# Kernel optimization log

Measured on AMD Instinct MI355X. Metric: run time of the kernel, lower is better.

Reference implementation:

```python
import math
import jax, jax.numpy as jnp
import numpy as np

D_MODEL, N_HEADS, D_FF = 2048, 16, 8192
B, T = 4, 1024
D_HEAD = D_MODEL // N_HEADS
LN_EPS = 1e-5


def hadamard(x):
    """Orthonormal Hadamard transform along last dim (power-of-two length)."""
    n = x.shape[-1]
    y = x.reshape(-1, n)
    h = 1
    while h < n:
        y = y.reshape(-1, n // (2 * h), 2, h)
        a, b = y[..., 0, :], y[..., 1, :]
        y = jnp.concatenate([a + b, a - b], axis=-1).reshape(-1, n)
        h *= 2
    return (y / math.sqrt(n)).reshape(x.shape)


def quantize_int8_per_row(W):
    s = jnp.maximum(jnp.max(jnp.abs(W), axis=1, keepdims=True), 1e-8) / 127.0
    Q = jnp.clip(jnp.round(W / s), -127, 127).astype(jnp.int8)
    return Q, s


def make_dtdr_weight(key, out_f, in_f):
    W = jax.random.normal(key, (out_f, in_f), dtype=jnp.float32) * 0.02
    return quantize_int8_per_row(hadamard(W))  # W_tilde = W @ H, then int8


def setup_inputs() -> dict:
    key = jax.random.key(0)
    ks = jax.random.split(key, 8)
    x = jax.random.normal(ks[0], (B, T, D_MODEL), dtype=jnp.float32)
    Qq, sq = make_dtdr_weight(ks[1], D_MODEL, D_MODEL)
    Qk, sk = make_dtdr_weight(ks[2], D_MODEL, D_MODEL)
    Qv, sv = make_dtdr_weight(ks[3], D_MODEL, D_MODEL)
    Qo, so = make_dtdr_weight(ks[4], D_MODEL, D_MODEL)
    Qf1, sf1 = make_dtdr_weight(ks[5], D_FF, D_MODEL)
    Qf2, sf2 = make_dtdr_weight(ks[6], D_MODEL, D_FF)
    return dict(
        x=x,
        ln1_g=jnp.ones((D_MODEL,), jnp.float32), ln1_b=jnp.zeros((D_MODEL,), jnp.float32),
        ln2_g=jnp.ones((D_MODEL,), jnp.float32), ln2_b=jnp.zeros((D_MODEL,), jnp.float32),
        Qq=Qq, sq=sq, Qk=Qk, sk=sk, Qv=Qv, sv=sv, Qo=Qo, so=so,
        Qf1=Qf1, sf1=sf1, bf1=jnp.zeros((D_FF,), jnp.float32),
        Qf2=Qf2, sf2=sf2, bf2=jnp.zeros((D_MODEL,), jnp.float32),
    )


def layernorm(x, g, b):
    mu = jnp.mean(x, axis=-1, keepdims=True)
    var = jnp.mean(jnp.square(x - mu), axis=-1, keepdims=True)
    return (x - mu) / jnp.sqrt(var + LN_EPS) * g + b


def dtdr_linear(x, Q, s, bias=None):
    # y = (H x) @ dequant(Q)^T + b
    xh = hadamard(x.astype(jnp.float32))
    W = Q.astype(jnp.float32) * s  # (out, in)
    y = jnp.einsum('btd,od->bto', xh, W)
    return y if bias is None else y + bias


def reference(x, ln1_g, ln1_b, ln2_g, ln2_b, Qq, sq, Qk, sk, Qv, sv, Qo, so,
              Qf1, sf1, bf1, Qf2, sf2, bf2):
    Bc, Tc, C = x.shape
    h = layernorm(x, ln1_g, ln1_b)
    q = dtdr_linear(h, Qq, sq).reshape(Bc, Tc, N_HEADS, D_HEAD).transpose(0, 2, 1, 3)
    k = dtdr_linear(h, Qk, sk).reshape(Bc, Tc, N_HEADS, D_HEAD).transpose(0, 2, 1, 3)
    v = dtdr_linear(h, Qv, sv).reshape(Bc, Tc, N_HEADS, D_HEAD).transpose(0, 2, 1, 3)
    scores = jnp.einsum('bhqd,bhkd->bhqk', q, k) / math.sqrt(D_HEAD)
    p = jax.nn.softmax(scores, axis=-1)
    out = jnp.einsum('bhqk,bhkd->bhqd', p, v)
    out = out.transpose(0, 2, 1, 3).reshape(Bc, Tc, C)
    x = x + dtdr_linear(out, Qo, so)
    h = layernorm(x, ln2_g, ln2_b)
    ff = dtdr_linear(h, Qf1, sf1, bf1)
    ff = jax.nn.gelu(ff, approximate=False)  # torch F.gelu default = erf gelu
    x = x + dtdr_linear(ff, Qf2, sf2, bf2)
    return x
```

## Files before the change

kernel.cpp:

```cpp
#include <hip/hip_runtime.h>
#include <cstdint>
#include <cstddef>

typedef unsigned short u16;
typedef unsigned int   u32;
typedef __bf16 bf16x8 __attribute__((ext_vector_type(8)));
typedef float  f32x4  __attribute__((ext_vector_type(4)));

__device__ __forceinline__ float bf2f(u16 u) {
  union { u32 i; float f; } v; v.i = ((u32)u) << 16; return v.f;
}
__device__ __forceinline__ u16 f2bf(float f) {
  union { float f; u32 i; } v; v.f = f;
  u32 r = v.i + 0x7fffu + ((v.i >> 16) & 1u);
  return (u16)(r >> 16);
}
__device__ __forceinline__ void unpack8(uint4 raw, float* v) {
  v[0]=bf2f(raw.x&0xffff); v[1]=bf2f(raw.x>>16);
  v[2]=bf2f(raw.y&0xffff); v[3]=bf2f(raw.y>>16);
  v[4]=bf2f(raw.z&0xffff); v[5]=bf2f(raw.z>>16);
  v[6]=bf2f(raw.w&0xffff); v[7]=bf2f(raw.w>>16);
}
__device__ __forceinline__ uint4 pack8(const float* v) {
  uint4 r;
  r.x = (u32)f2bf(v[0]) | ((u32)f2bf(v[1])<<16);
  r.y = (u32)f2bf(v[2]) | ((u32)f2bf(v[3])<<16);
  r.z = (u32)f2bf(v[4]) | ((u32)f2bf(v[5])<<16);
  r.w = (u32)f2bf(v[6]) | ((u32)f2bf(v[7])<<16);
  return r;
}
__device__ __forceinline__ void gload16(const void* g, void* l) {
  __builtin_amdgcn_global_load_lds((const __attribute__((address_space(1))) void*)g,
                                   (__attribute__((address_space(3))) void*)l, 16, 0, 0);
}

template<typename T>
__device__ __forceinline__ void load8(const T* p, float* v);
template<> __device__ __forceinline__ void load8<float>(const float* p, float* v) {
  const float4 a = ((const float4*)p)[0];
  const float4 b = ((const float4*)p)[1];
  v[0]=a.x; v[1]=a.y; v[2]=a.z; v[3]=a.w;
  v[4]=b.x; v[5]=b.y; v[6]=b.z; v[7]=b.w;
}
template<> __device__ __forceinline__ void load8<u16>(const u16* p, float* v) {
  unpack8(*(const uint4*)p, v);
}

__global__ __launch_bounds__(256) void cvt_k(const int* __restrict__ Q, u16* __restrict__ W) {
  const size_t i = ((size_t)blockIdx.x * 256 + threadIdx.x) * 8;
  const int4 a = *(const int4*)(Q + i);
  const int4 b = *(const int4*)(Q + i + 4);
  union { float f; u32 u; } c;
  uint4 r;
  u32 t;
  c.f = (float)a.x; t = c.u >> 16; c.f = (float)a.y; r.x = t | (c.u & 0xffff0000u);
  c.f = (float)a.z; t = c.u >> 16; c.f = (float)a.w; r.y = t | (c.u & 0xffff0000u);
  c.f = (float)b.x; t = c.u >> 16; c.f = (float)b.y; r.z = t | (c.u & 0xffff0000u);
  c.f = (float)b.z; t = c.u >> 16; c.f = (float)b.w; r.w = t | (c.u & 0xffff0000u);
  *(uint4*)(W + i) = r;
}

template<typename T>
__global__ __launch_bounds__(256) void ln_fwht_k(const T* __restrict__ X,
    const float* __restrict__ G, const float* __restrict__ Bt, u16* __restrict__ O) {
  __shared__ float buf[2048];
  __shared__ float red[8];
  const int tid = threadIdx.x;
  const int lane = tid & 63, wave = tid >> 6;
  const size_t base = (size_t)blockIdx.x * 2048;
  float v[8]; load8(X + base + tid*8, v);
  float s = 0.f, s2 = 0.f;
  for (int j = 0; j < 8; ++j) { s += v[j]; s2 += v[j]*v[j]; }
  for (int m = 1; m < 64; m <<= 1) { s += __shfl_xor(s, m, 64); s2 += __shfl_xor(s2, m, 64); }
  if (lane == 0) { red[wave] = s; red[4 + wave] = s2; }
  __syncthreads();
  s  = red[0] + red[1] + red[2] + red[3];
  s2 = red[4] + red[5] + red[6] + red[7];
  const float mu = s * (1.f/2048.f);
  const float rstd = rsqrtf(s2 * (1.f/2048.f) - mu*mu + 1e-5f);
  float g[8], bb[8];
  load8(G + tid*8, g); load8(Bt + tid*8, bb);
  for (int j = 0; j < 8; ++j) buf[tid*8 + j] = (v[j] - mu) * rstd * g[j] + bb[j];
  __syncthreads();
  for (int h = 1; h < 2048; h <<= 1) {
    for (int p = 0; p < 4; ++p) {
      const int idx = p*256 + tid;
      const int i = ((idx & ~(h-1)) << 1) | (idx & (h-1));
      const float a = buf[i], c = buf[i + h];
      buf[i] = a + c; buf[i + h] = a - c;
    }
    __syncthreads();
  }
  float o[8];
  for (int j = 0; j < 8; ++j) o[j] = buf[tid*8 + j] * 0.02209708691207961f;
  *(uint4*)&O[base + tid*8] = pack8(o);
}

template<int N>
__global__ __launch_bounds__(256) void fwht_ip(u16* __restrict__ D) {
  __shared__ float buf[N];
  const int tid = threadIdx.x;
  const size_t base = (size_t)blockIdx.x * N;
  constexpr int V8 = N / (8*256);
  for (int i = 0; i < V8; ++i) {
    uint4 raw = *(const uint4*)&D[base + (i*256 + tid)*8];
    float v[8]; unpack8(raw, v);
    for (int j = 0; j < 8; ++j) buf[(i*256 + tid)*8 + j] = v[j];
  }
  __syncthreads();
  constexpr int PAIRS = N / 2 / 256;
  for (int h = 1; h < N; h <<= 1) {
    for (int p = 0; p < PAIRS; ++p) {
      const int idx = p*256 + tid;
      const int i = ((idx & ~(h-1)) << 1) | (idx & (h-1));
      const float a = buf[i], c = buf[i + h];
      buf[i] = a + c; buf[i + h] = a - c;
    }
    __syncthreads();
  }
  const float sc = rsqrtf((float)N);
  for (int i = 0; i < V8; ++i) {
    float v[8];
    for (int j = 0; j < 8; ++j) v[j] = buf[(i*256 + tid)*8 + j] * sc;
    *(uint4*)&D[base + (i*256 + tid)*8] = pack8(v);
  }
}

__global__ __launch_bounds__(256, 2) void gemm_bt(
    const u16* __restrict__ A, const u16* __restrict__ Bw, const float* __restrict__ S,
    void* __restrict__ C, int ldc, int M, int N, int K,
    const float* __restrict__ bias, const float* __restrict__ resf,
    const u16* __restrict__ resb, int dogelu, int outf32)
{
  __shared__ alignas(16) u16 sA[2][128*32];
  __shared__ alignas(16) u16 sB[2][128*32];
  const int tid = threadIdx.x;
  const int lane = tid & 63, wave = tid >> 6;
  const int quad = lane >> 4, l16 = lane & 15;
  const int wm = wave & 1, wn = wave >> 1;
  const int nwg = gridDim.x * gridDim.y;
  int flat = blockIdx.y * gridDim.x + blockIdx.x;
  if ((nwg & 7) == 0) flat = (flat & 7) * (nwg >> 3) + (flat >> 3);
  const long tM = (long)(flat % gridDim.x) * 128;
  const long tN = (long)(flat / gridDim.x) * 128;
  const int sr = lane >> 2;
  const int scol = (lane & 3) * 8;
  const u16* a0 = A  + (size_t)(tM + wave*16      + sr)*K + scol;
  const u16* a1 = A  + (size_t)(tM + (wave+4)*16  + sr)*K + scol;
  const u16* b0 = Bw + (size_t)(tN + wave*16      + sr)*K + scol;
  const u16* b1 = Bw + (size_t)(tN + (wave+4)*16  + sr)*K + scol;

  auto stage = [&](int buf, int k0) {
    gload16(a0 + k0, &sA[buf][ wave   *512]);
    gload16(a1 + k0, &sA[buf][(wave+4)*512]);
    gload16(b0 + k0, &sB[buf][ wave   *512]);
    gload16(b1 + k0, &sB[buf][(wave+4)*512]);
  };

  f32x4 acc[4][4] = {};
  auto compute = [&](int buf) {
    bf16x8 af[4], bq[4];
#pragma unroll
    for (int t = 0; t < 4; ++t) af[t] = *(const bf16x8*)&sA[buf][(wm*64 + t*16 + l16)*32 + quad*8];
#pragma unroll
    for (int t = 0; t < 4; ++t) bq[t] = *(const bf16x8*)&sB[buf][(wn*64 + t*16 + l16)*32 + quad*8];
#pragma unroll
    for (int im = 0; im < 4; ++im)
#pragma unroll
      for (int in = 0; in < 4; ++in)
        acc[im][in] = __builtin_amdgcn_mfma_f32_16x16x32_bf16(af[im], bq[in], acc[im][in], 0, 0, 0);
  };

  const int nk = K >> 5;
  stage(0, 0);
  __syncthreads();
  int cur = 0;
  for (int t = 0; t < nk - 1; ++t) {
    stage(cur ^ 1, (t + 1) << 5);
    compute(cur);
    __syncthreads();
    cur ^= 1;
  }
  compute(cur);

#pragma unroll
  for (int in = 0; in < 4; ++in) {
    const long col = tN + wn*64 + in*16 + l16;
    const float sc = S[col];
    const float bv = bias ? bias[col] : 0.f;
#pragma unroll
    for (int im = 0; im < 4; ++im) {
      const long row0 = tM + wm*64 + im*16 + quad*4;
#pragma unroll
      for (int r = 0; r < 4; ++r) {
        float v = acc[im][in][r] * sc + bv;
        if (dogelu) v = 0.5f * v * (1.f + erff(v * 0.7071067811865475f));
        const size_t off = (size_t)(row0 + r)*ldc + col;
        if (resf) v += resf[off];
        if (resb) v += bf2f(resb[off]);
        if (outf32) ((float*)C)[off] = v;
        else        ((u16*)C)[off]   = f2bf(v);
      }
    }
  }
}

__global__ __launch_bounds__(256, 2) void attn_k(const u16* __restrict__ QKV, u16* __restrict__ O)
{
  __shared__ alignas(16) u16 sKV[16384];
  __shared__ alignas(16) u16 sP[16384];
  const int tid = threadIdx.x;
  const int lane = tid & 63, wave = tid >> 6;
  const int quad = lane >> 4, l16 = lane & 15;
  const int qt = blockIdx.x;
  const int bh = blockIdx.y;
  const int b = bh >> 4, h = bh & 15;
  const size_t rb = (size_t)b * 1024;
  const u16* Qg = QKV + (rb + (size_t)qt*128)*6144 + h*128;
  const u16* Kg = QKV + rb*6144 + 2048 + h*128;
  const u16* Vg = QKV + rb*6144 + 4096 + h*128;

  for (int c = 0; c < 8; ++c) {
    const int chunk = c*4 + wave;
    const int r = chunk*4 + quad;
    gload16(Qg + (size_t)r*6144 + l16*8, &sP[chunk*512]);
  }
  __syncthreads();
  bf16x8 aq[2][4];
  for (int im = 0; im < 2; ++im)
    for (int kk = 0; kk < 4; ++kk)
      aq[im][kk] = *(const bf16x8*)&sP[(wave*32 + im*16 + l16)*128 + kk*32 + quad*8];

  float mrun[2][4], lrun[2][4];
  f32x4 oacc[2][8] = {};
  for (int im = 0; im < 2; ++im)
    for (int r = 0; r < 4; ++r) { mrun[im][r] = -1e30f; lrun[im][r] = 0.f; }

  for (int kt = 0; kt < 8; ++kt) {
    __syncthreads();
    for (int c = 0; c < 8; ++c) {
      const int chunk = c*4 + wave;
      const int r = chunk*4 + quad;
      gload16(Kg + (size_t)(kt*128 + r)*6144 + l16*8, &sKV[chunk*512]);
    }
    __syncthreads();
    f32x4 sf[2][8] = {};
#pragma unroll
    for (int kk = 0; kk < 4; ++kk)
#pragma unroll
      for (int jn = 0; jn < 8; ++jn) {
        const bf16x8 bk = *(const bf16x8*)&sKV[(jn*16 + l16)*128 + kk*32 + quad*8];
        sf[0][jn] = __builtin_amdgcn_mfma_f32_16x16x32_bf16(aq[0][kk], bk, sf[0][jn], 0, 0, 0);
        sf[1][jn] = __builtin_amdgcn_mfma_f32_16x16x32_bf16(aq[1][kk], bk, sf[1][jn], 0, 0, 0);
      }
    const float scale = 0.08838834764831845f;
#pragma unroll
    for (int im = 0; im < 2; ++im)
#pragma unroll
      for (int r = 0; r < 4; ++r) {
        float mx = -1e30f;
        for (int jn = 0; jn < 8; ++jn) mx = fmaxf(mx, sf[im][jn][r] * scale);
        for (int m = 1; m < 16; m <<= 1) mx = fmaxf(mx, __shfl_xor(mx, m, 64));
        const float mold = mrun[im][r];
        const float mnew = fmaxf(mold, mx);
        const float alpha = __expf(mold - mnew);
        float ls = 0.f;
        for (int jn = 0; jn < 8; ++jn) {
          const float p = __expf(sf[im][jn][r] * scale - mnew);
          ls += p;
          sP[wave*4096 + (im*16 + quad*4 + r)*128 + jn*16 + l16] = f2bf(p);
        }
        for (int m = 1; m < 16; m <<= 1) ls += __shfl_xor(ls, m, 64);
        lrun[im][r] = lrun[im][r]*alpha + ls;
        mrun[im][r] = mnew;
        for (int od = 0; od < 8; ++od) oacc[im][od][r] *= alpha;
      }
    __syncthreads();
    for (int c = 0; c < 8; ++c) {
      const int chunk = c*256 + tid;
      const int kv = chunk >> 4;
      const int db = (chunk & 15) * 8;
      const uint4 raw = *(const uint4*)(Vg + (size_t)(kt*128 + kv)*6144 + db);
      const u32 w0[4] = {raw.x, raw.y, raw.z, raw.w};
      for (int j = 0; j < 4; ++j) {
        sKV[(db + 2*j  )*128 + kv] = (u16)(w0[j] & 0xffff);
        sKV[(db + 2*j+1)*128 + kv] = (u16)(w0[j] >> 16);
      }
    }
    __syncthreads();
#pragma unroll
    for (int kk = 0; kk < 4; ++kk) {
      const bf16x8 ap0 = *(const bf16x8*)&sP[wave*4096 + (     l16)*128 + kk*32 + quad*8];
      const bf16x8 ap1 = *(const bf16x8*)&sP[wave*4096 + (16 + l16)*128 + kk*32 + quad*8];
#pragma unroll
      for (int od = 0; od < 8; ++od) {
        const bf16x8 bv = *(const bf16x8*)&sKV[(od*16 + l16)*128 + kk*32 + quad*8];
        oacc[0][od] = __builtin_amdgcn_mfma_f32_16x16x32_bf16(ap0, bv, oacc[0][od], 0, 0, 0);
        oacc[1][od] = __builtin_amdgcn_mfma_f32_16x16x32_bf16(ap1, bv, oacc[1][od], 0, 0, 0);
      }
    }
  }
  for (int im = 0; im < 2; ++im)
    for (int r = 0; r < 4; ++r) {
      const float inv = 1.f / lrun[im][r];
      const size_t row = rb + (size_t)qt*128 + wave*32 + im*16 + quad*4 + r;
      for (int od = 0; od < 8; ++od)
        O[row*2048 + h*128 + od*16 + l16] = f2bf(oacc[im][od][r] * inv);
    }
}

extern "C" void kernel_launch(void* const* d_in, const int* in_sizes, int n_in,
                              void* d_out, int out_size, void* d_ws, size_t ws_size,
                              hipStream_t stream) {
  const float* x    = (const float*)d_in[0];
  const float* ln1g = (const float*)d_in[1];
  const float* ln1b = (const float*)d_in[2];
  const float* ln2g = (const float*)d_in[3];
  const float* ln2b = (const float*)d_in[4];
  const int* Qq  = (const int*)d_in[5];  const float* sq  = (const float*)d_in[6];
  const int* Qk  = (const int*)d_in[7];  const float* sk  = (const float*)d_in[8];
  const int* Qv  = (const int*)d_in[9];  const float* sv  = (const float*)d_in[10];
  const int* Qo  = (const int*)d_in[11]; const float* so  = (const float*)d_in[12];
  const int* Qf1 = (const int*)d_in[13]; const float* sf1 = (const float*)d_in[14];
  const float* bf1 = (const float*)d_in[15];
  const int* Qf2 = (const int*)d_in[16]; const float* sf2 = (const float*)d_in[17];
  const float* bf2 = (const float*)d_in[18];

  u16* XH  = (u16*)d_ws;
  u16* Wsl = XH + 8388608;
  u16* QKV = XH + 16777216;
  u16* FF  = XH + 16777216;
  u16* Wf2 = XH;
  float* Xout = (float*)d_out;
  if (ws_size < (size_t)100663296) return;

  ln_fwht_k<float><<<4096, 256, 0, stream>>>(x, ln1g, ln1b, XH);

  cvt_k<<<2048, 256, 0, stream>>>(Qq, Wsl);
  gemm_bt<<<dim3(32,16), 256, 0, stream>>>(XH, Wsl, sq, QKV + 0,    6144, 4096, 2048, 2048, nullptr, nullptr, nullptr, 0, 0);
  cvt_k<<<2048, 256, 0, stream>>>(Qk, Wsl);
  gemm_bt<<<dim3(32,16), 256, 0, stream>>>(XH, Wsl, sk, QKV + 2048, 6144, 4096, 2048, 2048, nullptr, nullptr, nullptr, 0, 0);
  cvt_k<<<2048, 256, 0, stream>>>(Qv, Wsl);
  gemm_bt<<<dim3(32,16), 256, 0, stream>>>(XH, Wsl, sv, QKV + 4096, 6144, 4096, 2048, 2048, nullptr, nullptr, nullptr, 0, 0);

  attn_k<<<dim3(8, 64), 256, 0, stream>>>(QKV, XH);

  fwht_ip<2048><<<4096, 256, 0, stream>>>(XH);

  cvt_k<<<2048, 256, 0, stream>>>(Qo, Wsl);
  gemm_bt<<<dim3(32,16), 256, 0, stream>>>(XH, Wsl, so, Xout, 2048, 4096, 2048, 2048, nullptr, x, nullptr, 0, 1);

  ln_fwht_k<float><<<4096, 256, 0, stream>>>(Xout, ln2g, ln2b, XH);

  cvt_k<<<4096, 256, 0, stream>>>(Qf1, Wsl);
  gemm_bt<<<dim3(32,32), 256, 0, stream>>>(XH, Wsl, sf1,        FF + 0,    8192, 4096, 4096, 2048, bf1,        nullptr, nullptr, 1, 0);
  cvt_k<<<4096, 256, 0, stream>>>(Qf1 + (size_t)4096*2048, Wsl);
  gemm_bt<<<dim3(32,32), 256, 0, stream>>>(XH, Wsl, sf1 + 4096, FF + 4096, 8192, 4096, 4096, 2048, bf1 + 4096, nullptr, nullptr, 1, 0);

  fwht_ip<8192><<<4096, 256, 0, stream>>>(FF);

  cvt_k<<<8192, 256, 0, stream>>>(Qf2, Wf2);
  gemm_bt<<<dim3(32,16), 256, 0, stream>>>(FF, Wf2, sf2, Xout, 2048, 4096, 2048, 8192, bf2, Xout, nullptr, 0, 1);
}
```

Baseline: 1.226 ms.

## Replace GEMM with 256x128 triple-buffered swizzled kernel and fuse QKV projections

```diff
diff --git a/kernel.cpp b/kernel.cpp
--- a/kernel.cpp
+++ b/kernel.cpp
@@ -58,6 +58,12 @@
   c.f = (float)b.x; t = c.u >> 16; c.f = (float)b.y; r.z = t | (c.u & 0xffff0000u);
   c.f = (float)b.z; t = c.u >> 16; c.f = (float)b.w; r.w = t | (c.u & 0xffff0000u);
   *(uint4*)(W + i) = r;
+}
+
+__global__ __launch_bounds__(256) void scat_k(const float* __restrict__ a,
+    const float* __restrict__ b, const float* __restrict__ c, float* __restrict__ o) {
+  const int i = blockIdx.x * 256 + threadIdx.x;
+  o[i] = (i < 2048) ? a[i] : (i < 4096 ? b[i - 2048] : c[i - 4096]);
 }
 
 template<typename T>
@@ -126,62 +132,75 @@
   }
 }
 
-__global__ __launch_bounds__(256, 2) void gemm_bt(
+__global__ __launch_bounds__(512, 1) void gemm256(
     const u16* __restrict__ A, const u16* __restrict__ Bw, const float* __restrict__ S,
     void* __restrict__ C, int ldc, int M, int N, int K,
     const float* __restrict__ bias, const float* __restrict__ resf,
     const u16* __restrict__ resb, int dogelu, int outf32)
 {
-  __shared__ alignas(16) u16 sA[2][128*32];
-  __shared__ alignas(16) u16 sB[2][128*32];
+  __shared__ alignas(16) u16 sA[3][256*64];
+  __shared__ alignas(16) u16 sB[3][128*64];
   const int tid = threadIdx.x;
   const int lane = tid & 63, wave = tid >> 6;
   const int quad = lane >> 4, l16 = lane & 15;
-  const int wm = wave & 1, wn = wave >> 1;
+  const int wm = wave & 3, wn = wave >> 2;
   const int nwg = gridDim.x * gridDim.y;
   int flat = blockIdx.y * gridDim.x + blockIdx.x;
   if ((nwg & 7) == 0) flat = (flat & 7) * (nwg >> 3) + (flat >> 3);
-  const long tM = (long)(flat % gridDim.x) * 128;
+  const long tM = (long)(flat % gridDim.x) * 256;
   const long tN = (long)(flat / gridDim.x) * 128;
-  const int sr = lane >> 2;
-  const int scol = (lane & 3) * 8;
-  const u16* a0 = A  + (size_t)(tM + wave*16      + sr)*K + scol;
-  const u16* a1 = A  + (size_t)(tM + (wave+4)*16  + sr)*K + scol;
-  const u16* b0 = Bw + (size_t)(tN + wave*16      + sr)*K + scol;
-  const u16* b1 = Bw + (size_t)(tN + (wave+4)*16  + sr)*K + scol;
+
+  const int rc = lane >> 3;
+  const int cswz = ((lane & 7) ^ rc) * 8;
+  const u16* Ab = A  + (size_t)(tM + rc) * K + cswz;
+  const u16* Bb = Bw + (size_t)(tN + rc) * K + cswz;
 
   auto stage = [&](int buf, int k0) {
-    gload16(a0 + k0, &sA[buf][ wave   *512]);
-    gload16(a1 + k0, &sA[buf][(wave+4)*512]);
-    gload16(b0 + k0, &sB[buf][ wave   *512]);
-    gload16(b1 + k0, &sB[buf][(wave+4)*512]);
+#pragma unroll
+    for (int i = 0; i < 4; ++i) {
+      const int chunk = i*8 + wave;
+      gload16(Ab + (size_t)(chunk*8)*K + k0, &sA[buf][chunk*512]);
+    }
+#pragma unroll
+    for (int i = 0; i < 2; ++i) {
+      const int chunk = i*8 + wave;
+      gload16(Bb + (size_t)(chunk*8)*K + k0, &sB[buf][chunk*512]);
+    }
   };
 
   f32x4 acc[4][4] = {};
   auto compute = [&](int buf) {
-    bf16x8 af[4], bq[4];
-#pragma unroll
-    for (int t = 0; t < 4; ++t) af[t] = *(const bf16x8*)&sA[buf][(wm*64 + t*16 + l16)*32 + quad*8];
-#pragma unroll
-    for (int t = 0; t < 4; ++t) bq[t] = *(const bf16x8*)&sB[buf][(wn*64 + t*16 + l16)*32 + quad*8];
-#pragma unroll
-    for (int im = 0; im < 4; ++im)
-#pragma unroll
-      for (int in = 0; in < 4; ++in)
-        acc[im][in] = __builtin_amdgcn_mfma_f32_16x16x32_bf16(af[im], bq[in], acc[im][in], 0, 0, 0);
+#pragma unroll
+    for (int ks = 0; ks < 2; ++ks) {
+      bf16x8 af[4], bq[4];
+      const int oc = ks*4 + quad;
+#pragma unroll
+      for (int mt = 0; mt < 4; ++mt)
+        af[mt] = *(const bf16x8*)&sA[buf][(wm*64 + mt*16 + l16)*64 + ((oc ^ (l16 & 7)))*8];
+#pragma unroll
+      for (int nt = 0; nt < 4; ++nt)
+        bq[nt] = *(const bf16x8*)&sB[buf][(wn*64 + nt*16 + l16)*64 + ((oc ^ (l16 & 7)))*8];
+      __builtin_amdgcn_s_setprio(1);
+#pragma unroll
+      for (int mt = 0; mt < 4; ++mt)
+#pragma unroll
+        for (int nt = 0; nt < 4; ++nt)
+          acc[mt][nt] = __builtin_amdgcn_mfma_f32_16x16x32_bf16(af[mt], bq[nt], acc[mt][nt], 0, 0, 0);
+      __builtin_amdgcn_s_setprio(0);
+    }
   };
 
-  const int nk = K >> 5;
+  const int ntk = K >> 6;
   stage(0, 0);
-  __syncthreads();
-  int cur = 0;
-  for (int t = 0; t < nk - 1; ++t) {
-    stage(cur ^ 1, (t + 1) << 5);
-    compute(cur);
-    __syncthreads();
-    cur ^= 1;
-  }
-  compute(cur);
+  if (ntk > 1) stage(1, 64);
+  for (int t = 0; t < ntk; ++t) {
+    if (t + 1 < ntk) { asm volatile("s_waitcnt vmcnt(6)" ::: "memory"); }
+    else             { asm volatile("s_waitcnt vmcnt(0)" ::: "memory"); }
+    __builtin_amdgcn_s_barrier();
+    __builtin_amdgcn_sched_barrier(0);
+    if (t + 2 < ntk) stage((t + 2) % 3, (t + 2) << 6);
+    compute(t % 3);
+  }
 
 #pragma unroll
   for (int in = 0; in < 4; ++in) {
@@ -326,39 +345,45 @@
   const int* Qf2 = (const int*)d_in[16]; const float* sf2 = (const float*)d_in[17];
   const float* bf2 = (const float*)d_in[18];
 
-  u16* XH  = (u16*)d_ws;
-  u16* Wsl = XH + 8388608;
-  u16* QKV = XH + 16777216;
-  u16* FF  = XH + 16777216;
-  u16* Wf2 = XH;
+  u16* XH   = (u16*)d_ws;
+  u16* Wq   = XH + 8388608;
+  u16* Wsl  = XH + 8388608;
+  u16* QKVb = XH + 20971520;
+  u16* FFb  = XH + 16777216;
+  u16* Wf2  = XH;
+  float* Scat = (float*)(XH + 46137344);
   float* Xout = (float*)d_out;
   if (ws_size < (size_t)100663296) return;
 
   ln_fwht_k<float><<<4096, 256, 0, stream>>>(x, ln1g, ln1b, XH);
 
-  cvt_k<<<2048, 256, 0, stream>>>(Qq, Wsl);
-  gemm_bt<<<dim3(32,16), 256, 0, stream>>>(XH, Wsl, sq, QKV + 0,    6144, 4096, 2048, 2048, nullptr, nullptr, nullptr, 0, 0);
-  cvt_k<<<2048, 256, 0, stream>>>(Qk, Wsl);
-  gemm_bt<<<dim3(32,16), 256, 0, stream>>>(XH, Wsl, sk, QKV + 2048, 6144, 4096, 2048, 2048, nullptr, nullptr, nullptr, 0, 0);
-  cvt_k<<<2048, 256, 0, stream>>>(Qv, Wsl);
-  gemm_bt<<<dim3(32,16), 256, 0, stream>>>(XH, Wsl, sv, QKV + 4096, 6144, 4096, 2048, 2048, nullptr, nullptr, nullptr, 0, 0);
-
-  attn_k<<<dim3(8, 64), 256, 0, stream>>>(QKV, XH);
+  cvt_k<<<2048, 256, 0, stream>>>(Qq, Wq);
+  cvt_k<<<2048, 256, 0, stream>>>(Qk, Wq + 4194304);
+  cvt_k<<<2048, 256, 0, stream>>>(Qv, Wq + 8388608);
+  scat_k<<<24, 256, 0, stream>>>(sq, sk, sv, Scat);
+  gemm256<<<dim3(16,48), 512, 0, stream>>>(XH, Wq, Scat, QKVb, 6144, 4096, 6144, 2048,
+                                           nullptr, nullptr, nullptr, 0, 0);
+
+  attn_k<<<dim3(8, 64), 256, 0, stream>>>(QKVb, XH);
 
   fwht_ip<2048><<<4096, 256, 0, stream>>>(XH);
 
   cvt_k<<<2048, 256, 0, stream>>>(Qo, Wsl);
-  gemm_bt<<<dim3(32,16), 256, 0, stream>>>(XH, Wsl, so, Xout, 2048, 4096, 2048, 2048, nullptr, x, nullptr, 0, 1);
+  gemm256<<<dim3(16,16), 512, 0, stream>>>(XH, Wsl, so, Xout, 2048, 4096, 2048, 2048,
+                                           nullptr, x, nullptr, 0, 1);
 
   ln_fwht_k<float><<<4096, 256, 0, stream>>>(Xout, ln2g, ln2b, XH);
 
   cvt_k<<<4096, 256, 0, stream>>>(Qf1, Wsl);
-  gemm_bt<<<dim3(32,32), 256, 0, stream>>>(XH, Wsl, sf1,        FF + 0,    8192, 4096, 4096, 2048, bf1,        nullptr, nullptr, 1, 0);
+  gemm256<<<dim3(16,32), 512, 0, stream>>>(XH, Wsl, sf1,        FFb + 0,    8192, 4096, 4096, 2048,
+                                           bf1,        nullptr, nullptr, 1, 0);
   cvt_k<<<4096, 256, 0, stream>>>(Qf1 + (size_t)4096*2048, Wsl);
-  gemm_bt<<<dim3(32,32), 256, 0, stream>>>(XH, Wsl, sf1 + 4096, FF + 4096, 8192, 4096, 4096, 2048, bf1 + 4096, nullptr, nullptr, 1, 0);
-
-  fwht_ip<8192><<<4096, 256, 0, stream>>>(FF);
+  gemm256<<<dim3(16,32), 512, 0, stream>>>(XH, Wsl, sf1 + 4096, FFb + 4096, 8192, 4096, 4096, 2048,
+                                           bf1 + 4096, nullptr, nullptr, 1, 0);
+
+  fwht_ip<8192><<<4096, 256, 0, stream>>>(FFb);
 
   cvt_k<<<8192, 256, 0, stream>>>(Qf2, Wf2);
-  gemm_bt<<<dim3(32,16), 256, 0, stream>>>(FF, Wf2, sf2, Xout, 2048, 4096, 2048, 8192, bf2, Xout, nullptr, 0, 1);
-}
+  gemm256<<<dim3(16,16), 512, 0, stream>>>(FFb, Wf2, sf2, Xout, 2048, 4096, 2048, 8192,
+                                           bf2, Xout, nullptr, 0, 1);
+}
```

Result: no change. 1.203 ms (-1.9%).
